# Kernel optimization log

Measured on AMD Instinct MI355X. Metric: run time of the kernel, lower is better.

The kernel has to match this reference:

```python
import jax, jax.numpy as jnp
import numpy as np

B, D, H, E, TOPK, NTASK = 16384, 128, 4, 8, 2, 1
ODIM = D // H  # MoE expert output dim (input_feat // num_heads)


def setup_inputs() -> dict:
    key = jax.random.key(0)
    ks = jax.random.split(key, 12)
    s = lambda k, shp, fan: jax.random.normal(k, shp, jnp.float32) / np.sqrt(fan)
    return {
        "x": jax.random.normal(ks[0], (B, D), jnp.float32),
        "Wq": s(ks[1], (D, D * H), D), "bq": jnp.zeros((D * H,), jnp.float32),
        "Wk": s(ks[2], (D, D * H), D), "bk": jnp.zeros((D * H,), jnp.float32),
        "Wg": s(ks[3], (D, E), D),
        "W1": s(ks[4], (E, D, D), D), "b1": jnp.zeros((E, D), jnp.float32),
        "W2": s(ks[5], (E, D, ODIM), D), "b2": jnp.zeros((E, ODIM), jnp.float32),
        "Wout": s(ks[6], (H * ODIM, NTASK), H * ODIM),
        "bout": jnp.zeros((NTASK,), jnp.float32),
    }


def reference(x, Wq, bq, Wk, bk, Wg, W1, b1, W2, b2, Wout, bout):
    # query/key projections -> [B, H, D] token views, flattened to [N, D]
    tok = (x @ Wq + bq).reshape(B * H, D)
    gate_tok = (x @ Wk + bk).reshape(B * H, D)

    # gating: softmax over experts, top-2 routing with renormalized weights
    probs = jax.nn.softmax(gate_tok @ Wg, axis=-1)          # [N, E]
    top_p, top_i = jax.lax.top_k(probs, TOPK)               # [N, k]
    weights = top_p / jnp.sum(top_p, axis=-1, keepdims=True)

    # expert MLPs (dense all-expert compute, then gather selected)
    h = jax.nn.relu(jnp.einsum('nd,edh->neh', tok, W1) + b1)  # [N, E, D]
    eo = jnp.einsum('neh,eho->neo', h, W2) + b2               # [N, E, ODIM]
    sel = jnp.take_along_axis(eo, top_i[:, :, None], axis=1)  # [N, k, ODIM]
    y = jnp.sum(weights[:, :, None] * sel, axis=1)            # [N, ODIM]

    # load-balancing auxiliary loss (switch-style): E * sum(frac_i * mean_prob_i)
    one_hot = jax.nn.one_hot(top_i[:, 0], E, dtype=probs.dtype)
    frac = jnp.mean(one_hot, axis=0)
    mean_p = jnp.mean(probs, axis=0)
    aux_loss = E * jnp.sum(frac * mean_p)

    out = y.reshape(B, H * ODIM) @ Wout + bout                # [B, NTASK]
    return out, aux_loss
```

## Files before the change

### kernel.cpp

```cpp
#include <hip/hip_runtime.h>
#include <hip/hip_bf16.h>

#define BB   16384
#define DD   128
#define HH   4
#define EE   8
#define NN   (BB*HH)
#define OD   32
#define PT   136

typedef __attribute__((ext_vector_type(8))) short short8;
typedef __attribute__((ext_vector_type(4))) short short4v;
typedef __attribute__((ext_vector_type(4))) float f32x4;

static __device__ __forceinline__ short f2bf(float v) {
    unsigned int u = __builtin_bit_cast(unsigned int, v);
    u = (u + 0x7FFFu + ((u >> 16) & 1u)) >> 16;
    return (short)u;
}

__global__ __launch_bounds__(256) void prep(
    const float* __restrict__ Wq, const float* __restrict__ Wk, const float* __restrict__ Wg,
    const float* __restrict__ bk, const float* __restrict__ W1, const float* __restrict__ W2,
    const float* __restrict__ bout,
    short* __restrict__ WqF, short* __restrict__ W1F, short* __restrict__ W2F,
    float* __restrict__ Wkg, float* __restrict__ bkg, float* __restrict__ out)
{
    int idx = blockIdx.x * 256 + threadIdx.x;
    if (idx < 65536) {
        int j = idx & 7, lane = (idx >> 3) & 63, ks = (idx >> 9) & 3, ct = idx >> 11;
        int l16 = lane & 15, quad = lane >> 4;
        int c = ct * 16 + l16, k = ks * 32 + quad * 8 + j;
        WqF[idx] = f2bf(Wq[k * 512 + c]);
    } else if (idx < 196608) {
        int r = idx - 65536;
        int j = r & 7, lane = (r >> 3) & 63, ks = (r >> 9) & 3, mt = (r >> 11) & 7, e = r >> 14;
        int l16 = lane & 15, quad = lane >> 4;
        int m = mt * 16 + l16, k = ks * 32 + quad * 8 + j;
        W1F[r] = f2bf(W1[e * 16384 + k * 128 + m]);
    } else if (idx < 229376) {
        int r = idx - 196608;
        int j = r & 7, lane = (r >> 3) & 63, ks = (r >> 9) & 3, mt = (r >> 11) & 1, e = r >> 12;
        int l16 = lane & 15, quad = lane >> 4;
        int m = mt * 16 + l16, k = ks * 32 + quad * 8 + j;
        W2F[r] = f2bf(W2[e * 4096 + k * 32 + m]);
    } else if (idx < 233472) {
        int r = idx - 229376;
        int k = r >> 5, col = r & 31, hh = col >> 3, e = col & 7;
        float s = 0.f;
        for (int d = 0; d < 128; ++d) s += Wk[k * 512 + hh * 128 + d] * Wg[d * 8 + e];
        Wkg[k * 32 + col] = s;
    } else if (idx < 233504) {
        int r = idx - 233472;
        int hh = r >> 3, e = r & 7;
        float s = 0.f;
        for (int d = 0; d < 128; ++d) s += bk[hh * 128 + d] * Wg[d * 8 + e];
        bkg[r] = s;
    } else if (idx < 249888) {
        out[idx - 233504] = bout[0];
    }
}

__global__ __launch_bounds__(256) void k1q_tok(
    const float* __restrict__ x, const short* __restrict__ WqF, const float* __restrict__ bq,
    short* __restrict__ tokb)
{
    __shared__ short xL[32 * PT];
    const int t  = threadIdx.x;
    const int b0 = blockIdx.x * 32;

    {
        int slot = t >> 3, seg = t & 7;
        const float4* src = (const float4*)(x + (size_t)(b0 + slot) * 128 + seg * 16);
        float4 v0 = src[0], v1 = src[1], v2 = src[2], v3 = src[3];
        short8 a, b;
        a[0]=f2bf(v0.x); a[1]=f2bf(v0.y); a[2]=f2bf(v0.z); a[3]=f2bf(v0.w);
        a[4]=f2bf(v1.x); a[5]=f2bf(v1.y); a[6]=f2bf(v1.z); a[7]=f2bf(v1.w);
        b[0]=f2bf(v2.x); b[1]=f2bf(v2.y); b[2]=f2bf(v2.z); b[3]=f2bf(v2.w);
        b[4]=f2bf(v3.x); b[5]=f2bf(v3.y); b[6]=f2bf(v3.z); b[7]=f2bf(v3.w);
        *(short8*)(xL + slot * PT + seg * 16)     = a;
        *(short8*)(xL + slot * PT + seg * 16 + 8) = b;
    }
    __syncthreads();

    const int wv   = t >> 6;
    const int lane = t & 63;
    const int l16  = lane & 15;
    const int quad = lane >> 4;

    f32x4 acc[8][2];
    #pragma unroll
    for (int ml = 0; ml < 8; ++ml)
        #pragma unroll
        for (int nl = 0; nl < 2; ++nl)
            acc[ml][nl] = (f32x4){0.f, 0.f, 0.f, 0.f};

    short8 bf[2][4];
    #pragma unroll
    for (int nl = 0; nl < 2; ++nl)
        #pragma unroll
        for (int ks = 0; ks < 4; ++ks)
            bf[nl][ks] = *(const short8*)(xL + (nl*16 + l16) * PT + ks*32 + quad*8);

    #pragma unroll
    for (int ks = 0; ks < 4; ++ks) {
        short8 af[8];
        #pragma unroll
        for (int ml = 0; ml < 8; ++ml)
            af[ml] = *(const short8*)(WqF + ((size_t)(((wv*8 + ml)*4 + ks)*64 + lane)) * 8);
        #pragma unroll
        for (int ml = 0; ml < 8; ++ml)
            #pragma unroll
            for (int nl = 0; nl < 2; ++nl)
                acc[ml][nl] = __builtin_amdgcn_mfma_f32_16x16x32_bf16(af[ml], bf[nl][ks], acc[ml][nl], 0, 0, 0);
    }

    #pragma unroll
    for (int ml = 0; ml < 8; ++ml) {
        int c0 = wv*128 + ml*16 + quad*4;
        f32x4 bqv = *(const f32x4*)(bq + c0);
        #pragma unroll
        for (int nl = 0; nl < 2; ++nl) {
            int b = b0 + nl*16 + l16;
            short4v hv;
            #pragma unroll
            for (int r = 0; r < 4; ++r) hv[r] = f2bf(acc[ml][nl][r] + bqv[r]);
            *(short4v*)(tokb + (size_t)b * 512 + c0) = hv;
        }
    }
}

__global__ __launch_bounds__(256) void k1_gate(
    const float* __restrict__ x, const float* __restrict__ Wkg, const float* __restrict__ bkg,
    int* __restrict__ topi, float* __restrict__ wts, float* __restrict__ blkPart)
{
    __shared__ float xL[64 * 129];
    __shared__ float lps[EE];
    __shared__ float lcn[EE];
    __shared__ float lasg[EE];

    const int t  = threadIdx.x;
    const int b0 = blockIdx.x * 64;

    if (t < EE) { lps[t] = 0.f; lcn[t] = 0.f; lasg[t] = 0.f; }

    for (int i = t; i < 2048; i += 256) {
        int r = i >> 5, c = i & 31;
        float4 v = ((const float4*)(x + (size_t)(b0 + r) * 128))[c];
        float* dst = xL + r * 129 + c * 4;
        dst[0] = v.x; dst[1] = v.y; dst[2] = v.z; dst[3] = v.w;
    }
    __syncthreads();

    const int h  = __builtin_amdgcn_readfirstlane(t >> 6);
    const int lb = t & 63;

    const f32x4* wkg4 = (const f32x4*)Wkg;
    f32x4 a0 = ((const f32x4*)bkg)[h * 2];
    f32x4 a1 = ((const f32x4*)bkg)[h * 2 + 1];

    const float* xrow = xL + lb * 129;
    #pragma unroll 4
    for (int k = 0; k < 128; ++k) {
        float xv = xrow[k];
        f32x4 w0 = wkg4[k * 8 + h * 2];
        f32x4 w1 = wkg4[k * 8 + h * 2 + 1];
        a0 += w0 * xv;
        a1 += w1 * xv;
    }

    float l[8] = {a0[0], a0[1], a0[2], a0[3], a1[0], a1[1], a1[2], a1[3]};
    float mx = l[0];
    #pragma unroll
    for (int e = 1; e < 8; ++e) mx = fmaxf(mx, l[e]);
    float p[8]; float sm = 0.f;
    #pragma unroll
    for (int e = 0; e < 8; ++e) { p[e] = __expf(l[e] - mx); sm += p[e]; }
    float isin = 1.f / sm;
    #pragma unroll
    for (int e = 0; e < 8; ++e) p[e] *= isin;

    int i1 = 0; float p1 = p[0];
    #pragma unroll
    for (int e = 1; e < 8; ++e) if (p[e] > p1) { p1 = p[e]; i1 = e; }
    int i2 = (i1 == 0) ? 1 : 0; float p2 = p[i2];
    #pragma unroll
    for (int e = 0; e < 8; ++e) if (e != i1 && p[e] > p2) { p2 = p[e]; i2 = e; }

    int n = (b0 + lb) * 4 + h;
    float rinv = 1.f / (p1 + p2);
    topi[2*n]   = i1;        topi[2*n+1] = i2;
    wts[2*n]    = p1 * rinv; wts[2*n+1]  = p2 * rinv;

    #pragma unroll
    for (int e = 0; e < 8; ++e) {
        float v = p[e];
        #pragma unroll
        for (int m2 = 1; m2 < 64; m2 <<= 1) v += __shfl_xor(v, m2);
        unsigned long long m1b = __ballot(i1 == e);
        unsigned long long m2b = __ballot(i2 == e);
        if (lb == 0) {
            float c1 = (float)__popcll(m1b);
            atomicAdd(&lps[e], v);
            atomicAdd(&lcn[e], c1);
            atomicAdd(&lasg[e], c1 + (float)__popcll(m2b));
        }
    }
    __syncthreads();
    if (t < EE) {
        float* bp = blkPart + blockIdx.x * 32;
        bp[t]      = lps[t];
        bp[8 + t]  = lcn[t];
        bp[16 + t] = lasg[t];
    }
}

__global__ __launch_bounds__(256) void k2s_scan(
    const float* __restrict__ blkPart,
    int* __restrict__ bases, int* __restrict__ cursors, int* __restrict__ assignCnt,
    float* __restrict__ out)
{
    __shared__ float red[8][32];
    __shared__ float fin[24];
    const int t = threadIdx.x;
    const int chunk = t >> 5, s = t & 31;
    float v = 0.f;
    for (int i = 0; i < 32; ++i) v += blkPart[(chunk * 32 + i) * 32 + s];
    red[chunk][s] = v;
    __syncthreads();
    if (t < 24) {
        float sum = 0.f;
        #pragma unroll
        for (int c = 0; c < 8; ++c) sum += red[c][t];
        fin[t] = sum;
    }
    __syncthreads();
    if (t == 0) {
        int b = 0;
        float aux = 0.f;
        const float invN = 1.f / (float)NN;
        for (int e = 0; e < EE; ++e) {
            aux += (fin[8 + e] * invN) * (fin[e] * invN);
            int a = (int)(fin[16 + e] + 0.5f);
            assignCnt[e] = a;
            bases[e] = b; cursors[e] = b;
            b += (a + 63) & ~63;
        }
        out[BB] = (float)EE * aux;
    }
}

__global__ __launch_bounds__(256) void k2a_bin(
    const int* __restrict__ topi,
    int* __restrict__ cursors, int* __restrict__ listIdx)
{
    __shared__ int lcnt[EE];
    __shared__ int lbase[EE];
    int t = threadIdx.x;
    if (t < EE) lcnt[t] = 0;
    __syncthreads();
    int n = blockIdx.x * 256 + t;
    int i0 = topi[2*n], i1 = topi[2*n+1];
    int s0 = atomicAdd(&lcnt[i0], 1);
    int s1 = atomicAdd(&lcnt[i1], 1);
    __syncthreads();
    if (t < EE) lbase[t] = atomicAdd(&cursors[t], lcnt[t]);
    __syncthreads();
    listIdx[lbase[i0] + s0] = 2*n;
    listIdx[lbase[i1] + s1] = 2*n + 1;
}

__global__ __launch_bounds__(256) void k2b_expert(
    const short* __restrict__ tokb, const short* __restrict__ W1F,
    const float* __restrict__ b1, const short* __restrict__ W2F, const float* __restrict__ b2,
    const int* __restrict__ assignCnt, const int* __restrict__ bases,
    const int* __restrict__ listIdx, const float* __restrict__ wts,
    const float* __restrict__ Wout, float* __restrict__ out)
{
    __shared__ short tokL[64 * PT];
    __shared__ short hL[64 * PT];
    __shared__ int   ids[64];
    __shared__ float wsl[64];
    __shared__ float WoutL[128];

    const int e    = blockIdx.y;
    const int cnt  = assignCnt[e];
    const int off  = blockIdx.x * 64;
    if (off >= cnt) return;
    const int sb   = bases[e] + off;
    const int t    = threadIdx.x;
    const int nt   = min(64, cnt - off);

    if (t < 64) {
        int a = listIdx[sb + min(t, nt - 1)];
        ids[t] = a >> 1;
        wsl[t] = (t < nt) ? wts[a] : 0.f;
    }
    if (t >= 128 && t < 256) WoutL[t - 128] = Wout[t - 128];
    __syncthreads();

    #pragma unroll
    for (int r = 0; r < 4; ++r) {
        int i = t + r * 256;
        int slot = i >> 4, seg = i & 15;
        short8 v = *(const short8*)(tokb + (size_t)ids[slot] * 128 + seg * 8);
        *(short8*)(tokL + slot * PT + seg * 8) = v;
    }
    __syncthreads();

    const int wv   = t >> 6;
    const int lane = t & 63;
    const int l16  = lane & 15;
    const int quad = lane >> 4;

    f32x4 acc[2][4];
    #pragma unroll
    for (int ml = 0; ml < 2; ++ml)
        #pragma unroll
        for (int nl = 0; nl < 4; ++nl)
            acc[ml][nl] = (f32x4){0.f, 0.f, 0.f, 0.f};

    short8 af[2][4];
    #pragma unroll
    for (int ml = 0; ml < 2; ++ml)
        #pragma unroll
        for (int ks = 0; ks < 4; ++ks)
            af[ml][ks] = *(const short8*)(W1F + ((size_t)(((e*8 + wv*2 + ml)*4 + ks)*64 + lane)) * 8);

    short8 bf[4][4];
    #pragma unroll
    for (int nl = 0; nl < 4; ++nl)
        #pragma unroll
        for (int ks = 0; ks < 4; ++ks)
            bf[nl][ks] = *(const short8*)(tokL + (nl*16 + l16) * PT + ks*32 + quad*8);

    #pragma unroll
    for (int ks = 0; ks < 4; ++ks)
        #pragma unroll
        for (int ml = 0; ml < 2; ++ml)
            #pragma unroll
            for (int nl = 0; nl < 4; ++nl)
                acc[ml][nl] = __builtin_amdgcn_mfma_f32_16x16x32_bf16(af[ml][ks], bf[nl][ks], acc[ml][nl], 0, 0, 0);

    #pragma unroll
    for (int ml = 0; ml < 2; ++ml) {
        int hid0 = wv*32 + ml*16 + quad*4;
        f32x4 b1v = *(const f32x4*)(b1 + e*128 + hid0);
        #pragma unroll
        for (int nl = 0; nl < 4; ++nl) {
            short4v hv;
            #pragma unroll
            for (int r = 0; r < 4; ++r) {
                float v = acc[ml][nl][r] + b1v[r];
                hv[r] = f2bf(fmaxf(v, 0.f));
            }
            *(short4v*)(hL + (nl*16 + l16) * PT + hid0) = hv;
        }
    }
    __syncthreads();

    f32x4 acc2[2];
    acc2[0] = (f32x4){0.f, 0.f, 0.f, 0.f};
    acc2[1] = (f32x4){0.f, 0.f, 0.f, 0.f};

    short8 af2[2][4];
    #pragma unroll
    for (int ml = 0; ml < 2; ++ml)
        #pragma unroll
        for (int ks = 0; ks < 4; ++ks)
            af2[ml][ks] = *(const short8*)(W2F + ((size_t)(((e*2 + ml)*4 + ks)*64 + lane)) * 8);

    short8 bf2[4];
    #pragma unroll
    for (int ks = 0; ks < 4; ++ks)
        bf2[ks] = *(const short8*)(hL + (wv*16 + l16) * PT + ks*32 + quad*8);

    #pragma unroll
    for (int ks = 0; ks < 4; ++ks)
        #pragma unroll
        for (int ml = 0; ml < 2; ++ml)
            acc2[ml] = __builtin_amdgcn_mfma_f32_16x16x32_bf16(af2[ml][ks], bf2[ks], acc2[ml], 0, 0, 0);

    const int slot = wv*16 + l16;
    const int nn   = ids[slot];
    const int hsel = nn & 3;
    float partial = 0.f;
    #pragma unroll
    for (int ml = 0; ml < 2; ++ml) {
        int od0 = ml*16 + quad*4;
        f32x4 b2v = *(const f32x4*)(b2 + e*32 + od0);
        const float* wseg = WoutL + hsel*32 + od0;
        #pragma unroll
        for (int r = 0; r < 4; ++r)
            partial += (acc2[ml][r] + b2v[r]) * wseg[r];
    }
    partial += __shfl_xor(partial, 16);
    partial += __shfl_xor(partial, 32);
    if (quad == 0) {
        float v = partial * wsl[slot];
        atomicAdd(&out[nn >> 2], v);
    }
}

extern "C" void kernel_launch(void* const* d_in, const int* in_sizes, int n_in,
                              void* d_out, int out_size, void* d_ws, size_t ws_size,
                              hipStream_t stream) {
    (void)in_sizes; (void)n_in; (void)out_size; (void)ws_size;
    const float* x    = (const float*)d_in[0];
    const float* Wq   = (const float*)d_in[1];
    const float* bq   = (const float*)d_in[2];
    const float* Wk   = (const float*)d_in[3];
    const float* bk   = (const float*)d_in[4];
    const float* Wg   = (const float*)d_in[5];
    const float* W1   = (const float*)d_in[6];
    const float* b1   = (const float*)d_in[7];
    const float* W2   = (const float*)d_in[8];
    const float* b2   = (const float*)d_in[9];
    const float* Wout = (const float*)d_in[10];
    const float* bout = (const float*)d_in[11];
    float* out = (float*)d_out;

    char* ws = (char*)d_ws;
    short* tokb     = (short*)(ws + 0);
    int*   topi     = (int*)  (ws + 16777216);
    float* wts      = (float*)(ws + 17301504);
    int*   listIdx  = (int*)  (ws + 17825792);
    short* WqF      = (short*)(ws + 18352128);
    short* W1F      = (short*)(ws + 18483200);
    short* W2F      = (short*)(ws + 18745344);
    float* Wkg      = (float*)(ws + 18810880);
    float* bkg      = (float*)(ws + 18827264);
    float* blkPart  = (float*)(ws + 18827392);
    int*   bases    = (int*)  (ws + 18860160);
    int*   cursors  = (int*)  (ws + 18860192);
    int*   assignCnt= (int*)  (ws + 18860224);

    prep<<<977, 256, 0, stream>>>(Wq, Wk, Wg, bk, W1, W2, bout, WqF, W1F, W2F, Wkg, bkg, out);
    k1q_tok<<<512, 256, 0, stream>>>(x, WqF, bq, tokb);
    k1_gate<<<256, 256, 0, stream>>>(x, Wkg, bkg, topi, wts, blkPart);
    k2s_scan<<<1, 256, 0, stream>>>(blkPart, bases, cursors, assignCnt, out);
    k2a_bin<<<256, 256, 0, stream>>>(topi, cursors, listIdx);
    k2b_expert<<<dim3(1024, 8), 256, 0, stream>>>(tokb, W1F, b1, W2F, b2, assignCnt, bases, listIdx, wts, Wout, out);
}
```

Before: 138.6 us.

## Fuse query projection, gating and scan into one kernel; compact expert grid

Merges the query-projection kernel, the gating kernel and the single-block scan into one kernel. It reuses the x tile already loaded into shared memory and picks the last-finishing block with an atomic done-counter to do the final reduction. The expert kernel now launches a 1D grid of exactly the needed tiles and maps each tile to its expert with a small prefix loop, so far fewer empty blocks exit early. This removes two launches and a redundant read of x. In exchange, half the lanes of each wave sit idle during gating, and the last-block pattern depends on threadfence ordering.

New measurement: 147.7 us. +6.5%, slower.

```diff
diff --git a/kernel.cpp b/kernel.cpp
--- a/kernel.cpp
+++ b/kernel.cpp
@@ -8,6 +8,8 @@
 #define NN   (BB*HH)
 #define OD   32
 #define PT   136
+#define GATE_PT 132
+#define NBLK 512
 
 typedef __attribute__((ext_vector_type(8))) short short8;
 typedef __attribute__((ext_vector_type(4))) short short4v;
@@ -24,7 +26,8 @@
     const float* __restrict__ bk, const float* __restrict__ W1, const float* __restrict__ W2,
     const float* __restrict__ bout,
     short* __restrict__ WqF, short* __restrict__ W1F, short* __restrict__ W2F,
-    float* __restrict__ Wkg, float* __restrict__ bkg, float* __restrict__ out)
+    float* __restrict__ Wkg, float* __restrict__ bkg, float* __restrict__ out,
+    int* __restrict__ doneCnt)
 {
     int idx = blockIdx.x * 256 + threadIdx.x;
     if (idx < 65536) {
@@ -58,21 +61,37 @@
         bkg[r] = s;
     } else if (idx < 249888) {
         out[idx - 233504] = bout[0];
-    }
-}
-
-__global__ __launch_bounds__(256) void k1q_tok(
+    } else if (idx == 249888) {
+        *doneCnt = 0;
+    }
+}
+
+__global__ __launch_bounds__(256) void k1qg(
     const float* __restrict__ x, const short* __restrict__ WqF, const float* __restrict__ bq,
-    short* __restrict__ tokb)
+    const float* __restrict__ Wkg, const float* __restrict__ bkg,
+    short* __restrict__ tokb, int* __restrict__ topi, float* __restrict__ wts,
+    float* __restrict__ blkPart, int* __restrict__ doneCnt,
+    int* __restrict__ bases, int* __restrict__ cursors, int* __restrict__ assignCnt,
+    int* __restrict__ totalTiles, float* __restrict__ out)
 {
     __shared__ short xL[32 * PT];
+    __shared__ float xF[32 * GATE_PT];
+    __shared__ float lps[EE], lcn[EE], lasg[EE];
+    __shared__ float red[8][32];
+    __shared__ float fin[24];
+    __shared__ int   isLast;
+
     const int t  = threadIdx.x;
     const int b0 = blockIdx.x * 32;
+
+    if (t < EE) { lps[t] = 0.f; lcn[t] = 0.f; lasg[t] = 0.f; }
 
     {
         int slot = t >> 3, seg = t & 7;
         const float4* src = (const float4*)(x + (size_t)(b0 + slot) * 128 + seg * 16);
         float4 v0 = src[0], v1 = src[1], v2 = src[2], v3 = src[3];
+        float4* fdst = (float4*)(xF + slot * GATE_PT + seg * 16);
+        fdst[0] = v0; fdst[1] = v1; fdst[2] = v2; fdst[3] = v3;
         short8 a, b;
         a[0]=f2bf(v0.x); a[1]=f2bf(v0.y); a[2]=f2bf(v0.z); a[3]=f2bf(v0.w);
         a[4]=f2bf(v1.x); a[5]=f2bf(v1.y); a[6]=f2bf(v1.z); a[7]=f2bf(v1.w);
@@ -88,122 +107,101 @@
     const int l16  = lane & 15;
     const int quad = lane >> 4;
 
-    f32x4 acc[8][2];
-    #pragma unroll
-    for (int ml = 0; ml < 8; ++ml)
+    {
+        f32x4 acc[8][2];
+        #pragma unroll
+        for (int ml = 0; ml < 8; ++ml)
+            #pragma unroll
+            for (int nl = 0; nl < 2; ++nl)
+                acc[ml][nl] = (f32x4){0.f, 0.f, 0.f, 0.f};
+
+        short8 bf[2][4];
         #pragma unroll
         for (int nl = 0; nl < 2; ++nl)
-            acc[ml][nl] = (f32x4){0.f, 0.f, 0.f, 0.f};
-
-    short8 bf[2][4];
-    #pragma unroll
-    for (int nl = 0; nl < 2; ++nl)
-        #pragma unroll
-        for (int ks = 0; ks < 4; ++ks)
-            bf[nl][ks] = *(const short8*)(xL + (nl*16 + l16) * PT + ks*32 + quad*8);
-
-    #pragma unroll
-    for (int ks = 0; ks < 4; ++ks) {
-        short8 af[8];
-        #pragma unroll
-        for (int ml = 0; ml < 8; ++ml)
-            af[ml] = *(const short8*)(WqF + ((size_t)(((wv*8 + ml)*4 + ks)*64 + lane)) * 8);
-        #pragma unroll
-        for (int ml = 0; ml < 8; ++ml)
-            #pragma unroll
-            for (int nl = 0; nl < 2; ++nl)
-                acc[ml][nl] = __builtin_amdgcn_mfma_f32_16x16x32_bf16(af[ml], bf[nl][ks], acc[ml][nl], 0, 0, 0);
-    }
-
-    #pragma unroll
-    for (int ml = 0; ml < 8; ++ml) {
-        int c0 = wv*128 + ml*16 + quad*4;
-        f32x4 bqv = *(const f32x4*)(bq + c0);
-        #pragma unroll
-        for (int nl = 0; nl < 2; ++nl) {
-            int b = b0 + nl*16 + l16;
-            short4v hv;
-            #pragma unroll
-            for (int r = 0; r < 4; ++r) hv[r] = f2bf(acc[ml][nl][r] + bqv[r]);
-            *(short4v*)(tokb + (size_t)b * 512 + c0) = hv;
+            #pragma unroll
+            for (int ks = 0; ks < 4; ++ks)
+                bf[nl][ks] = *(const short8*)(xL + (nl*16 + l16) * PT + ks*32 + quad*8);
+
+        #pragma unroll
+        for (int ks = 0; ks < 4; ++ks) {
+            short8 af[8];
+            #pragma unroll
+            for (int ml = 0; ml < 8; ++ml)
+                af[ml] = *(const short8*)(WqF + ((size_t)(((wv*8 + ml)*4 + ks)*64 + lane)) * 8);
+            #pragma unroll
+            for (int ml = 0; ml < 8; ++ml)
+                #pragma unroll
+                for (int nl = 0; nl < 2; ++nl)
+                    acc[ml][nl] = __builtin_amdgcn_mfma_f32_16x16x32_bf16(af[ml], bf[nl][ks], acc[ml][nl], 0, 0, 0);
         }
-    }
-}
-
-__global__ __launch_bounds__(256) void k1_gate(
-    const float* __restrict__ x, const float* __restrict__ Wkg, const float* __restrict__ bkg,
-    int* __restrict__ topi, float* __restrict__ wts, float* __restrict__ blkPart)
-{
-    __shared__ float xL[64 * 129];
-    __shared__ float lps[EE];
-    __shared__ float lcn[EE];
-    __shared__ float lasg[EE];
-
-    const int t  = threadIdx.x;
-    const int b0 = blockIdx.x * 64;
-
-    if (t < EE) { lps[t] = 0.f; lcn[t] = 0.f; lasg[t] = 0.f; }
-
-    for (int i = t; i < 2048; i += 256) {
-        int r = i >> 5, c = i & 31;
-        float4 v = ((const float4*)(x + (size_t)(b0 + r) * 128))[c];
-        float* dst = xL + r * 129 + c * 4;
-        dst[0] = v.x; dst[1] = v.y; dst[2] = v.z; dst[3] = v.w;
-    }
-    __syncthreads();
-
-    const int h  = __builtin_amdgcn_readfirstlane(t >> 6);
-    const int lb = t & 63;
-
-    const f32x4* wkg4 = (const f32x4*)Wkg;
-    f32x4 a0 = ((const f32x4*)bkg)[h * 2];
-    f32x4 a1 = ((const f32x4*)bkg)[h * 2 + 1];
-
-    const float* xrow = xL + lb * 129;
-    #pragma unroll 4
-    for (int k = 0; k < 128; ++k) {
-        float xv = xrow[k];
-        f32x4 w0 = wkg4[k * 8 + h * 2];
-        f32x4 w1 = wkg4[k * 8 + h * 2 + 1];
-        a0 += w0 * xv;
-        a1 += w1 * xv;
-    }
-
-    float l[8] = {a0[0], a0[1], a0[2], a0[3], a1[0], a1[1], a1[2], a1[3]};
-    float mx = l[0];
-    #pragma unroll
-    for (int e = 1; e < 8; ++e) mx = fmaxf(mx, l[e]);
-    float p[8]; float sm = 0.f;
-    #pragma unroll
-    for (int e = 0; e < 8; ++e) { p[e] = __expf(l[e] - mx); sm += p[e]; }
-    float isin = 1.f / sm;
-    #pragma unroll
-    for (int e = 0; e < 8; ++e) p[e] *= isin;
-
-    int i1 = 0; float p1 = p[0];
-    #pragma unroll
-    for (int e = 1; e < 8; ++e) if (p[e] > p1) { p1 = p[e]; i1 = e; }
-    int i2 = (i1 == 0) ? 1 : 0; float p2 = p[i2];
-    #pragma unroll
-    for (int e = 0; e < 8; ++e) if (e != i1 && p[e] > p2) { p2 = p[e]; i2 = e; }
-
-    int n = (b0 + lb) * 4 + h;
-    float rinv = 1.f / (p1 + p2);
-    topi[2*n]   = i1;        topi[2*n+1] = i2;
-    wts[2*n]    = p1 * rinv; wts[2*n+1]  = p2 * rinv;
-
-    #pragma unroll
-    for (int e = 0; e < 8; ++e) {
-        float v = p[e];
-        #pragma unroll
-        for (int m2 = 1; m2 < 64; m2 <<= 1) v += __shfl_xor(v, m2);
-        unsigned long long m1b = __ballot(i1 == e);
-        unsigned long long m2b = __ballot(i2 == e);
-        if (lb == 0) {
-            float c1 = (float)__popcll(m1b);
-            atomicAdd(&lps[e], v);
-            atomicAdd(&lcn[e], c1);
-            atomicAdd(&lasg[e], c1 + (float)__popcll(m2b));
+
+        #pragma unroll
+        for (int ml = 0; ml < 8; ++ml) {
+            int c0 = wv*128 + ml*16 + quad*4;
+            f32x4 bqv = *(const f32x4*)(bq + c0);
+            #pragma unroll
+            for (int nl = 0; nl < 2; ++nl) {
+                int b = b0 + nl*16 + l16;
+                short4v hv;
+                #pragma unroll
+                for (int r = 0; r < 4; ++r) hv[r] = f2bf(acc[ml][nl][r] + bqv[r]);
+                *(short4v*)(tokb + (size_t)b * 512 + c0) = hv;
+            }
+        }
+    }
+
+    {
+        const int h   = __builtin_amdgcn_readfirstlane(wv);
+        const int row = lane;
+        if (row < 32) {
+            const f32x4* wkg4 = (const f32x4*)Wkg;
+            f32x4 a0 = ((const f32x4*)bkg)[h * 2];
+            f32x4 a1 = ((const f32x4*)bkg)[h * 2 + 1];
+            const float* xrow = xF + row * GATE_PT;
+            #pragma unroll 4
+            for (int k = 0; k < 128; ++k) {
+                float xv = xrow[k];
+                a0 += wkg4[k * 8 + h * 2]     * xv;
+                a1 += wkg4[k * 8 + h * 2 + 1] * xv;
+            }
+
+            float l[8] = {a0[0], a0[1], a0[2], a0[3], a1[0], a1[1], a1[2], a1[3]};
+            float mx = l[0];
+            #pragma unroll
+            for (int e = 1; e < 8; ++e) mx = fmaxf(mx, l[e]);
+            float p[8]; float sm = 0.f;
+            #pragma unroll
+            for (int e = 0; e < 8; ++e) { p[e] = __expf(l[e] - mx); sm += p[e]; }
+            float isin = 1.f / sm;
+            #pragma unroll
+            for (int e = 0; e < 8; ++e) p[e] *= isin;
+
+            int i1 = 0; float p1 = p[0];
+            #pragma unroll
+            for (int e = 1; e < 8; ++e) if (p[e] > p1) { p1 = p[e]; i1 = e; }
+            int i2 = (i1 == 0) ? 1 : 0; float p2 = p[i2];
+            #pragma unroll
+            for (int e = 0; e < 8; ++e) if (e != i1 && p[e] > p2) { p2 = p[e]; i2 = e; }
+
+            int n = (b0 + row) * 4 + h;
+            float rinv = 1.f / (p1 + p2);
+            topi[2*n]   = i1;        topi[2*n+1] = i2;
+            wts[2*n]    = p1 * rinv; wts[2*n+1]  = p2 * rinv;
+
+            #pragma unroll
+            for (int e = 0; e < 8; ++e) {
+                float v = p[e];
+                #pragma unroll
+                for (int m2 = 1; m2 < 32; m2 <<= 1) v += __shfl_xor(v, m2);
+                unsigned long long m1b = __ballot(i1 == e);
+                unsigned long long m2b = __ballot(i2 == e);
+                if (row == 0) {
+                    float c1 = (float)__popcll(m1b);
+                    atomicAdd(&lps[e], v);
+                    atomicAdd(&lcn[e], c1);
+                    atomicAdd(&lasg[e], c1 + (float)__popcll(m2b));
+                }
+            }
         }
     }
     __syncthreads();
@@ -213,20 +211,23 @@
         bp[8 + t]  = lcn[t];
         bp[16 + t] = lasg[t];
     }
-}
-
-__global__ __launch_bounds__(256) void k2s_scan(
-    const float* __restrict__ blkPart,
-    int* __restrict__ bases, int* __restrict__ cursors, int* __restrict__ assignCnt,
-    float* __restrict__ out)
-{
-    __shared__ float red[8][32];
-    __shared__ float fin[24];
-    const int t = threadIdx.x;
-    const int chunk = t >> 5, s = t & 31;
-    float v = 0.f;
-    for (int i = 0; i < 32; ++i) v += blkPart[(chunk * 32 + i) * 32 + s];
-    red[chunk][s] = v;
+    __syncthreads();
+
+    if (t == 0) {
+        __threadfence();
+        int prev = atomicAdd(doneCnt, 1);
+        isLast = (prev == NBLK - 1) ? 1 : 0;
+    }
+    __syncthreads();
+    if (!isLast) return;
+    __threadfence();
+
+    {
+        const int chunk = t >> 5, s = t & 31;
+        float v = 0.f;
+        for (int i = 0; i < 64; ++i) v += blkPart[(chunk * 64 + i) * 32 + s];
+        red[chunk][s] = v;
+    }
     __syncthreads();
     if (t < 24) {
         float sum = 0.f;
@@ -246,6 +247,7 @@
             bases[e] = b; cursors[e] = b;
             b += (a + 63) & ~63;
         }
+        totalTiles[0] = b >> 6;
         out[BB] = (float)EE * aux;
     }
 }
@@ -274,6 +276,7 @@
     const short* __restrict__ tokb, const short* __restrict__ W1F,
     const float* __restrict__ b1, const short* __restrict__ W2F, const float* __restrict__ b2,
     const int* __restrict__ assignCnt, const int* __restrict__ bases,
+    const int* __restrict__ totalTiles,
     const int* __restrict__ listIdx, const float* __restrict__ wts,
     const float* __restrict__ Wout, float* __restrict__ out)
 {
@@ -283,13 +286,20 @@
     __shared__ float wsl[64];
     __shared__ float WoutL[128];
 
-    const int e    = blockIdx.y;
-    const int cnt  = assignCnt[e];
-    const int off  = blockIdx.x * 64;
-    if (off >= cnt) return;
-    const int sb   = bases[e] + off;
-    const int t    = threadIdx.x;
-    const int nt   = min(64, cnt - off);
+    const int tile = blockIdx.x;
+    if (tile >= totalTiles[0]) return;
+
+    int e = 0, off = 0, cum = 0;
+    #pragma unroll
+    for (int i = 0; i < EE; ++i) {
+        int ti = (assignCnt[i] + 63) >> 6;
+        if (tile >= cum && tile < cum + ti) { e = i; off = (tile - cum) * 64; }
+        cum += ti;
+    }
+    const int cnt = assignCnt[e];
+    const int sb  = bases[e] + off;
+    const int t   = threadIdx.x;
+    const int nt  = min(64, cnt - off);
 
     if (t < 64) {
         int a = listIdx[sb + min(t, nt - 1)];
@@ -431,14 +441,18 @@
     float* Wkg      = (float*)(ws + 18810880);
     float* bkg      = (float*)(ws + 18827264);
     float* blkPart  = (float*)(ws + 18827392);
-    int*   bases    = (int*)  (ws + 18860160);
-    int*   cursors  = (int*)  (ws + 18860192);
-    int*   assignCnt= (int*)  (ws + 18860224);
-
-    prep<<<977, 256, 0, stream>>>(Wq, Wk, Wg, bk, W1, W2, bout, WqF, W1F, W2F, Wkg, bkg, out);
-    k1q_tok<<<512, 256, 0, stream>>>(x, WqF, bq, tokb);
-    k1_gate<<<256, 256, 0, stream>>>(x, Wkg, bkg, topi, wts, blkPart);
-    k2s_scan<<<1, 256, 0, stream>>>(blkPart, bases, cursors, assignCnt, out);
+    int*   bases    = (int*)  (ws + 18892928);
+    int*   cursors  = (int*)  (ws + 18892960);
+    int*   assignCnt= (int*)  (ws + 18892992);
+    int*   doneCnt  = (int*)  (ws + 18893024);
+    int*   totalTiles=(int*)  (ws + 18893028);
+
+    prep<<<977, 256, 0, stream>>>(Wq, Wk, Wg, bk, W1, W2, bout,
+                                  WqF, W1F, W2F, Wkg, bkg, out, doneCnt);
+    k1qg<<<NBLK, 256, 0, stream>>>(x, WqF, bq, Wkg, bkg, tokb, topi, wts,
+                                   blkPart, doneCnt, bases, cursors, assignCnt,
+                                   totalTiles, out);
     k2a_bin<<<256, 256, 0, stream>>>(topi, cursors, listIdx);
-    k2b_expert<<<dim3(1024, 8), 256, 0, stream>>>(tokb, W1F, b1, W2F, b2, assignCnt, bases, listIdx, wts, Wout, out);
-}
+    k2b_expert<<<2056, 256, 0, stream>>>(tokb, W1F, b1, W2F, b2, assignCnt, bases,
+                                         totalTiles, listIdx, wts, Wout, out);
+}
```

## Fuse scan and binning into gate kernel with per-expert fixed-stride lists

Applied to the files above, without the earlier changes.

The separate scan and binning kernels are folded into the gate kernel. Each block now atomically reserves slots in per-expert lists that have a fixed stride of NN entries, and the last block to finish (tracked by a done counter) computes the aux loss. This removes two kernel launches and the topi round-trip through global memory. In exchange the listIdx buffer grows, and the order of entries within each expert list is no longer deterministic.

After: 143.1 us. 1.03x slower.

```diff
diff --git a/kernel.cpp b/kernel.cpp
--- a/kernel.cpp
+++ b/kernel.cpp
@@ -8,6 +8,7 @@
 #define NN   (BB*HH)
 #define OD   32
 #define PT   136
+#define GNB  256
 
 typedef __attribute__((ext_vector_type(8))) short short8;
 typedef __attribute__((ext_vector_type(4))) short short4v;
@@ -24,7 +25,8 @@
     const float* __restrict__ bk, const float* __restrict__ W1, const float* __restrict__ W2,
     const float* __restrict__ bout,
     short* __restrict__ WqF, short* __restrict__ W1F, short* __restrict__ W2F,
-    float* __restrict__ Wkg, float* __restrict__ bkg, float* __restrict__ out)
+    float* __restrict__ Wkg, float* __restrict__ bkg, float* __restrict__ out,
+    int* __restrict__ cursors, int* __restrict__ doneCnt)
 {
     int idx = blockIdx.x * 256 + threadIdx.x;
     if (idx < 65536) {
@@ -58,6 +60,10 @@
         bkg[r] = s;
     } else if (idx < 249888) {
         out[idx - 233504] = bout[0];
+    } else if (idx < 249896) {
+        cursors[idx - 249888] = 0;
+    } else if (idx == 249896) {
+        *doneCnt = 0;
     }
 }
 
@@ -132,17 +138,20 @@
 
 __global__ __launch_bounds__(256) void k1_gate(
     const float* __restrict__ x, const float* __restrict__ Wkg, const float* __restrict__ bkg,
-    int* __restrict__ topi, float* __restrict__ wts, float* __restrict__ blkPart)
+    float* __restrict__ wts, int* __restrict__ listIdx, int* __restrict__ cursors,
+    float* __restrict__ blkPart, int* __restrict__ doneCnt, float* __restrict__ out)
 {
     __shared__ float xL[64 * 129];
-    __shared__ float lps[EE];
-    __shared__ float lcn[EE];
-    __shared__ float lasg[EE];
+    __shared__ float lps[EE], lcn[EE];
+    __shared__ int   lcnt[EE], lbase[EE];
+    __shared__ float red[8][16];
+    __shared__ float fin[16];
+    __shared__ int   isLast;
 
     const int t  = threadIdx.x;
     const int b0 = blockIdx.x * 64;
 
-    if (t < EE) { lps[t] = 0.f; lcn[t] = 0.f; lasg[t] = 0.f; }
+    if (t < EE) { lps[t] = 0.f; lcn[t] = 0.f; lcnt[t] = 0; }
 
     for (int i = t; i < 2048; i += 256) {
         int r = i >> 5, c = i & 31;
@@ -163,10 +172,8 @@
     #pragma unroll 4
     for (int k = 0; k < 128; ++k) {
         float xv = xrow[k];
-        f32x4 w0 = wkg4[k * 8 + h * 2];
-        f32x4 w1 = wkg4[k * 8 + h * 2 + 1];
-        a0 += w0 * xv;
-        a1 += w1 * xv;
+        a0 += wkg4[k * 8 + h * 2]     * xv;
+        a1 += wkg4[k * 8 + h * 2 + 1] * xv;
     }
 
     float l[8] = {a0[0], a0[1], a0[2], a0[3], a1[0], a1[1], a1[2], a1[3]};
@@ -187,10 +194,13 @@
     #pragma unroll
     for (int e = 0; e < 8; ++e) if (e != i1 && p[e] > p2) { p2 = p[e]; i2 = e; }
 
-    int n = (b0 + lb) * 4 + h;
+    const int n = (b0 + lb) * 4 + h;
     float rinv = 1.f / (p1 + p2);
-    topi[2*n]   = i1;        topi[2*n+1] = i2;
-    wts[2*n]    = p1 * rinv; wts[2*n+1]  = p2 * rinv;
+    wts[2*n]   = p1 * rinv;
+    wts[2*n+1] = p2 * rinv;
+
+    int s0 = atomicAdd(&lcnt[i1], 1);
+    int s1 = atomicAdd(&lcnt[i2], 1);
 
     #pragma unroll
     for (int e = 0; e < 8; ++e) {
@@ -198,37 +208,41 @@
         #pragma unroll
         for (int m2 = 1; m2 < 64; m2 <<= 1) v += __shfl_xor(v, m2);
         unsigned long long m1b = __ballot(i1 == e);
-        unsigned long long m2b = __ballot(i2 == e);
         if (lb == 0) {
-            float c1 = (float)__popcll(m1b);
             atomicAdd(&lps[e], v);
-            atomicAdd(&lcn[e], c1);
-            atomicAdd(&lasg[e], c1 + (float)__popcll(m2b));
+            atomicAdd(&lcn[e], (float)__popcll(m1b));
         }
     }
     __syncthreads();
+
+    if (t < EE) lbase[t] = atomicAdd(&cursors[t], lcnt[t]);
     if (t < EE) {
         float* bp = blkPart + blockIdx.x * 32;
-        bp[t]      = lps[t];
-        bp[8 + t]  = lcn[t];
-        bp[16 + t] = lasg[t];
-    }
-}
-
-__global__ __launch_bounds__(256) void k2s_scan(
-    const float* __restrict__ blkPart,
-    int* __restrict__ bases, int* __restrict__ cursors, int* __restrict__ assignCnt,
-    float* __restrict__ out)
-{
-    __shared__ float red[8][32];
-    __shared__ float fin[24];
-    const int t = threadIdx.x;
-    const int chunk = t >> 5, s = t & 31;
-    float v = 0.f;
-    for (int i = 0; i < 32; ++i) v += blkPart[(chunk * 32 + i) * 32 + s];
-    red[chunk][s] = v;
-    __syncthreads();
-    if (t < 24) {
+        bp[t]     = lps[t];
+        bp[8 + t] = lcn[t];
+    }
+    __syncthreads();
+
+    listIdx[i1 * NN + lbase[i1] + s0] = 2 * n;
+    listIdx[i2 * NN + lbase[i2] + s1] = 2 * n + 1;
+
+    if (t == 0) {
+        __threadfence();
+        int prev = atomicAdd(doneCnt, 1);
+        isLast = (prev == GNB - 1) ? 1 : 0;
+    }
+    __syncthreads();
+    if (!isLast) return;
+    __threadfence();
+
+    if (t < 128) {
+        const int chunk = t >> 4, s = t & 15;
+        float v = 0.f;
+        for (int i = 0; i < 32; ++i) v += blkPart[(chunk * 32 + i) * 32 + s];
+        red[chunk][s] = v;
+    }
+    __syncthreads();
+    if (t < 16) {
         float sum = 0.f;
         #pragma unroll
         for (int c = 0; c < 8; ++c) sum += red[c][t];
@@ -236,46 +250,19 @@
     }
     __syncthreads();
     if (t == 0) {
-        int b = 0;
         float aux = 0.f;
         const float invN = 1.f / (float)NN;
-        for (int e = 0; e < EE; ++e) {
+        for (int e = 0; e < EE; ++e)
             aux += (fin[8 + e] * invN) * (fin[e] * invN);
-            int a = (int)(fin[16 + e] + 0.5f);
-            assignCnt[e] = a;
-            bases[e] = b; cursors[e] = b;
-            b += (a + 63) & ~63;
-        }
         out[BB] = (float)EE * aux;
     }
-}
-
-__global__ __launch_bounds__(256) void k2a_bin(
-    const int* __restrict__ topi,
-    int* __restrict__ cursors, int* __restrict__ listIdx)
-{
-    __shared__ int lcnt[EE];
-    __shared__ int lbase[EE];
-    int t = threadIdx.x;
-    if (t < EE) lcnt[t] = 0;
-    __syncthreads();
-    int n = blockIdx.x * 256 + t;
-    int i0 = topi[2*n], i1 = topi[2*n+1];
-    int s0 = atomicAdd(&lcnt[i0], 1);
-    int s1 = atomicAdd(&lcnt[i1], 1);
-    __syncthreads();
-    if (t < EE) lbase[t] = atomicAdd(&cursors[t], lcnt[t]);
-    __syncthreads();
-    listIdx[lbase[i0] + s0] = 2*n;
-    listIdx[lbase[i1] + s1] = 2*n + 1;
 }
 
 __global__ __launch_bounds__(256) void k2b_expert(
     const short* __restrict__ tokb, const short* __restrict__ W1F,
     const float* __restrict__ b1, const short* __restrict__ W2F, const float* __restrict__ b2,
-    const int* __restrict__ assignCnt, const int* __restrict__ bases,
-    const int* __restrict__ listIdx, const float* __restrict__ wts,
-    const float* __restrict__ Wout, float* __restrict__ out)
+    const int* __restrict__ cursors, const int* __restrict__ listIdx,
+    const float* __restrict__ wts, const float* __restrict__ Wout, float* __restrict__ out)
 {
     __shared__ short tokL[64 * PT];
     __shared__ short hL[64 * PT];
@@ -284,10 +271,10 @@
     __shared__ float WoutL[128];
 
     const int e    = blockIdx.y;
-    const int cnt  = assignCnt[e];
+    const int cnt  = cursors[e];
     const int off  = blockIdx.x * 64;
     if (off >= cnt) return;
-    const int sb   = bases[e] + off;
+    const int sb   = e * NN + off;
     const int t    = threadIdx.x;
     const int nt   = min(64, cnt - off);
 
@@ -422,23 +409,22 @@
 
     char* ws = (char*)d_ws;
     short* tokb     = (short*)(ws + 0);
-    int*   topi     = (int*)  (ws + 16777216);
-    float* wts      = (float*)(ws + 17301504);
-    int*   listIdx  = (int*)  (ws + 17825792);
-    short* WqF      = (short*)(ws + 18352128);
-    short* W1F      = (short*)(ws + 18483200);
-    short* W2F      = (short*)(ws + 18745344);
-    float* Wkg      = (float*)(ws + 18810880);
-    float* bkg      = (float*)(ws + 18827264);
-    float* blkPart  = (float*)(ws + 18827392);
-    int*   bases    = (int*)  (ws + 18860160);
-    int*   cursors  = (int*)  (ws + 18860192);
-    int*   assignCnt= (int*)  (ws + 18860224);
-
-    prep<<<977, 256, 0, stream>>>(Wq, Wk, Wg, bk, W1, W2, bout, WqF, W1F, W2F, Wkg, bkg, out);
+    float* wts      = (float*)(ws + 16777216);
+    int*   listIdx  = (int*)  (ws + 17301504);
+    short* WqF      = (short*)(ws + 19398656);
+    short* W1F      = (short*)(ws + 19529728);
+    short* W2F      = (short*)(ws + 19791872);
+    float* Wkg      = (float*)(ws + 19857408);
+    float* bkg      = (float*)(ws + 19873792);
+    float* blkPart  = (float*)(ws + 19873920);
+    int*   cursors  = (int*)  (ws + 19906688);
+    int*   doneCnt  = (int*)  (ws + 19906720);
+
+    prep<<<977, 256, 0, stream>>>(Wq, Wk, Wg, bk, W1, W2, bout,
+                                  WqF, W1F, W2F, Wkg, bkg, out, cursors, doneCnt);
     k1q_tok<<<512, 256, 0, stream>>>(x, WqF, bq, tokb);
-    k1_gate<<<256, 256, 0, stream>>>(x, Wkg, bkg, topi, wts, blkPart);
-    k2s_scan<<<1, 256, 0, stream>>>(blkPart, bases, cursors, assignCnt, out);
-    k2a_bin<<<256, 256, 0, stream>>>(topi, cursors, listIdx);
-    k2b_expert<<<dim3(1024, 8), 256, 0, stream>>>(tokb, W1F, b1, W2F, b2, assignCnt, bases, listIdx, wts, Wout, out);
-}
+    k1_gate<<<GNB, 256, 0, stream>>>(x, Wkg, bkg, wts, listIdx, cursors,
+                                     blkPart, doneCnt, out);
+    k2b_expert<<<dim3(1024, 8), 256, 0, stream>>>(tokb, W1F, b1, W2F, b2,
+                                                  cursors, listIdx, wts, Wout, out);
+}
```
